# Optimization experiments

Hardware: AMD Instinct MI355X
Metric: run time of the kernel (lower is better)

The kernel has to match this reference:

```python
import jax, jax.numpy as jnp
import numpy as np

NEG_SLOPE = 0.01  # F.leaky_relu default
BN_EPS = 1e-5


def _nnconv_bn_lrelu(x, src, dst, ef, W_edge, b_edge, W_root, b_root, gamma, beta):
    # PyG NNConv (aggr='add'): msg_e = x_src[e] @ reshape(nn(edge_feat[e]), [in, out])
    E = ef.shape[0]
    in_c = x.shape[1]
    out_c = W_root.shape[1]
    We = (ef @ W_edge.T + b_edge).reshape(E, in_c, out_c)   # [E, in, out]
    msg = jnp.einsum('ei,eio->eo', x[src], We)               # gather + per-edge matvec
    aggr = jax.ops.segment_sum(msg, dst, num_segments=x.shape[0])  # scatter-add
    h = aggr + x @ W_root + b_root
    # BatchNorm1d in training mode: batch statistics over nodes (biased var)
    mean = jnp.mean(h, axis=0)
    var = jnp.var(h, axis=0)
    hn = (h - mean) * jax.lax.rsqrt(var + BN_EPS) * gamma + beta
    return jnp.where(hn > 0, hn, NEG_SLOPE * hn)             # LeakyReLU


def setup_inputs() -> dict:
    key = jax.random.key(0)
    ks = jax.random.split(key, 12)
    N, E = 8192, 32768
    D_NODE, D_EDGE, H, OUT = 64, 64, 64, 128
    node_features = jax.random.normal(ks[0], (N, D_NODE), dtype=jnp.float32)
    edge_index = jax.random.randint(ks[1], (2, E), 0, N, dtype=jnp.int32)
    edge_features = jax.random.normal(ks[2], (E, D_EDGE), dtype=jnp.float32)
    batch = jnp.zeros((N,), dtype=jnp.int32)
    s = 0.05
    params = {
        # layer 0: node_feats=D_NODE, edge_feats=D_EDGE, out=H
        'W_edge0': jax.random.normal(ks[3], (D_NODE * H, D_EDGE), dtype=jnp.float32) * s,
        'b_edge0': jnp.zeros((D_NODE * H,), dtype=jnp.float32),
        'W_root0': jax.random.normal(ks[4], (D_NODE, H), dtype=jnp.float32) * s,
        'b_root0': jnp.zeros((H,), dtype=jnp.float32),
        'gamma0': jnp.ones((H,), dtype=jnp.float32),
        'beta0': jnp.zeros((H,), dtype=jnp.float32),
        # layer 1: node_feats=H, edge_feats=H(==D_EDGE), out=H
        'W_edge1': jax.random.normal(ks[5], (H * H, D_EDGE), dtype=jnp.float32) * s,
        'b_edge1': jnp.zeros((H * H,), dtype=jnp.float32),
        'W_root1': jax.random.normal(ks[6], (H, H), dtype=jnp.float32) * s,
        'b_root1': jnp.zeros((H,), dtype=jnp.float32),
        'gamma1': jnp.ones((H,), dtype=jnp.float32),
        'beta1': jnp.zeros((H,), dtype=jnp.float32),
        # final linear
        'W_lin': jax.random.normal(ks[7], (OUT, H), dtype=jnp.float32) * s,
        'b_lin': jnp.zeros((OUT,), dtype=jnp.float32),
    }
    return {'node_features': node_features, 'edge_index': edge_index,
            'edge_features': edge_features, 'batch': batch, **params}


def reference(node_features, edge_index, edge_features, batch,
              W_edge0, b_edge0, W_root0, b_root0, gamma0, beta0,
              W_edge1, b_edge1, W_root1, b_root1, gamma1, beta1,
              W_lin, b_lin):
    src, dst = edge_index[0], edge_index[1]
    h = _nnconv_bn_lrelu(node_features, src, dst, edge_features,
                         W_edge0, b_edge0, W_root0, b_root0, gamma0, beta0)
    h = _nnconv_bn_lrelu(h, src, dst, edge_features,
                         W_edge1, b_edge1, W_root1, b_root1, gamma1, beta1)
    # dropout treated as identity (eval-mode determinism)
    return h @ W_lin.T + b_lin
```

## Files before the change

kernel.cpp:

```cpp
#include <hip/hip_runtime.h>

typedef __bf16 bf16x8 __attribute__((ext_vector_type(8)));
typedef float f32x4 __attribute__((ext_vector_type(4)));

#define NEG_SLOPE 0.01f
#define BN_EPS 1e-5f

static __device__ __forceinline__ unsigned short f2bf(float f) {
    unsigned u = __builtin_bit_cast(unsigned, f);
    unsigned r = (u + 0x7fffu + ((u >> 16) & 1u)) >> 16;
    return (unsigned short)r;
}
static __device__ __forceinline__ float bf2f(unsigned short s) {
    return __builtin_bit_cast(float, (unsigned)s << 16);
}
static __device__ __forceinline__ float lrelu(float v) {
    return fmaxf(v, 0.f) + NEG_SLOPE * fminf(v, 0.f);
}
static __device__ __forceinline__ f32x4 bn4(f32x4 v, f32x4 sc, f32x4 sh) {
    f32x4 r = v * sc + sh;
    r.x = lrelu(r.x); r.y = lrelu(r.y); r.z = lrelu(r.z); r.w = lrelu(r.w);
    return r;
}

__global__ __launch_bounds__(256) void prep(const float* __restrict__ We0,
                                            const float* __restrict__ We1,
                                            unsigned short* __restrict__ wbs0,
                                            unsigned short* __restrict__ wbs1,
                                            float* __restrict__ stats,
                                            const int* __restrict__ dst,
                                            int* __restrict__ hist, int E) {
    const int idx = blockIdx.x * 256 + threadIdx.x;
    if (blockIdx.x == 0) stats[threadIdx.x] = 0.f;
    if (idx < 65536) {
        const int t = idx;
        const float* We = (t >> 15) ? We1 : We0;
        unsigned short* wbs = (t >> 15) ? wbs1 : wbs0;
        const int r = t & 32767;
        const int i = r >> 9, os = (r >> 7) & 3, h = (r >> 6) & 1, l = r & 63;
        const float* sp = We + (size_t)(i * 64 + 16 * os + (l & 15)) * 64
                             + h * 32 + 8 * (l >> 4);
        const f32x4 v0 = *reinterpret_cast<const f32x4*>(sp);
        const f32x4 v1 = *reinterpret_cast<const f32x4*>(sp + 4);
        ushort4 u0, u1;
        u0.x = f2bf(v0.x); u0.y = f2bf(v0.y); u0.z = f2bf(v0.z); u0.w = f2bf(v0.w);
        u1.x = f2bf(v1.x); u1.y = f2bf(v1.y); u1.z = f2bf(v1.z); u1.w = f2bf(v1.w);
        *reinterpret_cast<ushort4*>(wbs + (size_t)r * 8) = u0;
        *reinterpret_cast<ushort4*>(wbs + (size_t)r * 8 + 4) = u1;
    } else {
        const int e = idx - 65536;
        if (e < E) atomicAdd(&hist[dst[e]], 1);
    }
}

__global__ __launch_bounds__(256) void scan_kernel(const int* __restrict__ hist,
                                                   int* __restrict__ ofs,
                                                   int* __restrict__ cur, int N) {
    __shared__ int wsum[4];
    const int tid = threadIdx.x;
    const int per = N / 256;
    const int base = tid * per;
    int loc[32];
    int s = 0;
#pragma unroll
    for (int k = 0; k < 32; ++k) { loc[k] = s; s += hist[base + k]; }
    const int lane = tid & 63, w = tid >> 6;
    int run = s;
#pragma unroll
    for (int d = 1; d < 64; d <<= 1) {
        int up = __shfl_up(run, d, 64);
        if (lane >= d) run += up;
    }
    const int excl = run - s;
    if (lane == 63) wsum[w] = run;
    __syncthreads();
    int woff = 0;
#pragma unroll
    for (int i = 0; i < 4; ++i) woff += (i < w) ? wsum[i] : 0;
    if (tid == 255) ofs[N] = woff + run;
    const int off = woff + excl;
#pragma unroll
    for (int k = 0; k < 32; ++k) {
        ofs[base + k] = off + loc[k];
        cur[base + k] = off + loc[k];
    }
}

__global__ __launch_bounds__(256) void scatter_reorder(
    const int* __restrict__ dst, const int* __restrict__ src,
    const float* __restrict__ ef, int* __restrict__ cur,
    unsigned short* __restrict__ ef_bs, int* __restrict__ src_s) {
    const int e = blockIdx.x * 256 + threadIdx.x;
    const int p = atomicAdd(&cur[dst[e]], 1);
    src_s[p] = src[e];
    const float* er = ef + (size_t)e * 64;
    unsigned short* orow = ef_bs + (size_t)p * 64;
#pragma unroll
    for (int c = 0; c < 16; ++c) {
        const f32x4 v = *reinterpret_cast<const f32x4*>(er + 4 * c);
        ushort4 u;
        u.x = f2bf(v.x); u.y = f2bf(v.y); u.z = f2bf(v.z); u.w = f2bf(v.w);
        *reinterpret_cast<ushort4*>(orow + 4 * c) = u;
    }
}

__global__ __launch_bounds__(256) void node_mm2(
    const float* __restrict__ x,
    const float* __restrict__ Wr, const float* __restrict__ br,
    const float* __restrict__ be,
    float* __restrict__ aggr, float* __restrict__ NB,
    const float* __restrict__ sums, const float* __restrict__ gamma,
    const float* __restrict__ beta, float invN) {
    __shared__ float Ml[64][64];
    __shared__ float Bl[64][64];
    __shared__ float xl[64][64];
    __shared__ float ssl[128];
    const int tid = threadIdx.x;
    if (sums) {
        if (tid < 64) {
            const float mean = sums[tid] * invN;
            const float var  = sums[64 + tid] * invN - mean * mean;
            const float sc = gamma[tid] * rsqrtf(var + BN_EPS);
            ssl[tid] = sc;
            ssl[64 + tid] = beta[tid] - mean * sc;
        }
        __syncthreads();
    }
    const int n0 = blockIdx.x * 64;
    for (int f = tid; f < 1024; f += 256) {
        int r = f >> 4, c = f & 15;
        *reinterpret_cast<float4*>(&Ml[r][c * 4]) =
            *reinterpret_cast<const float4*>(Wr + (size_t)r * 64 + c * 4);
        *reinterpret_cast<float4*>(&Bl[r][c * 4]) =
            *reinterpret_cast<const float4*>(be + (size_t)r * 64 + c * 4);
        f32x4 xv = *reinterpret_cast<const f32x4*>(x + (size_t)(n0 + r) * 64 + c * 4);
        if (sums) {
            const f32x4 sc = *reinterpret_cast<const f32x4*>(&ssl[c * 4]);
            const f32x4 sh = *reinterpret_cast<const f32x4*>(&ssl[64 + c * 4]);
            xv = bn4(xv, sc, sh);
        }
        *reinterpret_cast<f32x4*>(&xl[r][c * 4]) = xv;
    }
    __syncthreads();
    const int o = tid & 63, g = tid >> 6;
    float accA[16] = {}, accB[16] = {};
    for (int i4 = 0; i4 < 16; ++i4) {
        float m0 = Ml[4 * i4 + 0][o], m1 = Ml[4 * i4 + 1][o];
        float m2 = Ml[4 * i4 + 2][o], m3 = Ml[4 * i4 + 3][o];
        float b0 = Bl[4 * i4 + 0][o], b1 = Bl[4 * i4 + 1][o];
        float b2 = Bl[4 * i4 + 2][o], b3 = Bl[4 * i4 + 3][o];
#pragma unroll
        for (int k = 0; k < 16; ++k) {
            const f32x4 xv = *reinterpret_cast<const f32x4*>(&xl[g + 4 * k][4 * i4]);
            accA[k] += xv.x * m0 + xv.y * m1 + xv.z * m2 + xv.w * m3;
            accB[k] += xv.x * b0 + xv.y * b1 + xv.z * b2 + xv.w * b3;
        }
    }
    const float b = br[o];
#pragma unroll
    for (int k = 0; k < 16; ++k) {
        aggr[(size_t)(n0 + g + 4 * k) * 64 + o] = accA[k] + b;
        NB[(size_t)(n0 + g + 4 * k) * 64 + o]   = accB[k];
    }
}

__global__ __launch_bounds__(512, 1) void msg_fused(
    const unsigned short* __restrict__ ef_bs,
    const unsigned short* __restrict__ wbs,
    const float* __restrict__ x,
    const float* __restrict__ NB,
    const int* __restrict__ src_s,
    unsigned short* __restrict__ msg,
    const float* __restrict__ sums, const float* __restrict__ gamma,
    const float* __restrict__ beta, float invN) {
    __shared__ unsigned short wlds[32768];
    __shared__ float xT2[8192];
    __shared__ float ssl[128];
    const int tid = threadIdx.x;
    const int e0 = blockIdx.x * 128;
    if (sums) {
        if (tid < 64) {
            const float mean = sums[tid] * invN;
            const float var  = sums[64 + tid] * invN - mean * mean;
            const float sc = gamma[tid] * rsqrtf(var + BN_EPS);
            ssl[tid] = sc;
            ssl[64 + tid] = beta[tid] - mean * sc;
        }
        __syncthreads();
    }

#pragma unroll
    for (int it = 0; it < 4; ++it) {
        int f = it * 512 + tid;
        int e = f & 127, c = f >> 7;
        int s = src_s[e0 + e];
        f32x4 xv = *reinterpret_cast<const f32x4*>(x + (size_t)s * 64 + c * 4);
        if (sums) {
            const f32x4 sc = *reinterpret_cast<const f32x4*>(&ssl[c * 4]);
            const f32x4 sh = *reinterpret_cast<const f32x4*>(&ssl[64 + c * 4]);
            xv = bn4(xv, sc, sh);
        }
        const int base = (e >> 6) * 64 + (e & 15) * 4 + ((e >> 4) & 3);
        xT2[(4 * c + 0) * 128 + base] = xv.x;
        xT2[(4 * c + 1) * 128 + base] = xv.y;
        xT2[(4 * c + 2) * 128 + base] = xv.z;
        xT2[(4 * c + 3) * 128 + base] = xv.w;
    }

    const int w = tid >> 6, l = tid & 63, lg = l >> 4, ln = l & 15;
    const int os = w & 3, eh = w >> 2;

    bf16x8 B0[4], B1[4];
#pragma unroll
    for (int tt = 0; tt < 4; ++tt) {
        const unsigned short* pe = ef_bs + (size_t)(e0 + 64 * eh + 16 * tt + ln) * 64 + 8 * lg;
        B0[tt] = *reinterpret_cast<const bf16x8*>(pe);
        B1[tt] = *reinterpret_cast<const bf16x8*>(pe + 32);
    }

    const char* gW = (const char*)wbs;
    char* wldsB = (char*)wlds;
#define GLD(c, j) (*reinterpret_cast<const bf16x8*>(gW + (size_t)(c) * 32768 + (j) * 8192 + tid * 16))
#define SST(b, j, v) (*reinterpret_cast<bf16x8*>(wldsB + (b) * 32768 + (j) * 8192 + tid * 16) = (v))

    bf16x8 S0 = GLD(0, 0), S1 = GLD(0, 1), S2 = GLD(0, 2), S3 = GLD(0, 3);
    SST(0, 0, S0); SST(0, 1, S1); SST(0, 2, S2); SST(0, 3, S3);
    S0 = GLD(1, 0); S1 = GLD(1, 1); S2 = GLD(1, 2); S3 = GLD(1, 3);
    __syncthreads();

    f32x4 acc[4] = {};
    const int wofs = os * 1024 + l * 8;
    for (int t = 0; t < 16; ++t) {
        const unsigned short* wb_ = wlds + (t & 1) * 16384 + wofs;
#pragma unroll
        for (int ii = 0; ii < 4; ++ii) {
            const bf16x8 A0 = *reinterpret_cast<const bf16x8*>(wb_ + ii * 4096);
            const bf16x8 A1 = *reinterpret_cast<const bf16x8*>(wb_ + ii * 4096 + 512);
            const f32x4 xs = *reinterpret_cast<const f32x4*>(
                &xT2[(t * 4 + ii) * 128 + eh * 64 + ln * 4]);
#pragma unroll
            for (int tt = 0; tt < 4; ++tt) {
                f32x4 c = {};
                c = __builtin_amdgcn_mfma_f32_16x16x32_bf16(A0, B0[tt], c, 0, 0, 0);
                c = __builtin_amdgcn_mfma_f32_16x16x32_bf16(A1, B1[tt], c, 0, 0, 0);
                acc[tt] += xs[tt] * c;
            }
        }
        if (t < 15) {
            const int nb = (t + 1) & 1;
            SST(nb, 0, S0); SST(nb, 1, S1); SST(nb, 2, S2); SST(nb, 3, S3);
            if (t < 14) {
                S0 = GLD(t + 2, 0); S1 = GLD(t + 2, 1);
                S2 = GLD(t + 2, 2); S3 = GLD(t + 2, 3);
            }
        }
        __syncthreads();
    }
#undef GLD
#undef SST

#pragma unroll
    for (int tt = 0; tt < 4; ++tt) {
        const int e = e0 + 64 * eh + 16 * tt + ln;
        const int s = src_s[e];
        const f32x4 nbv = *reinterpret_cast<const f32x4*>(NB + (size_t)s * 64 + os * 16 + 4 * lg);
        const f32x4 add = acc[tt] + nbv;
        ushort4 u;
        u.x = f2bf(add.x); u.y = f2bf(add.y); u.z = f2bf(add.z); u.w = f2bf(add.w);
        *reinterpret_cast<ushort4*>(msg + (size_t)e * 64 + os * 16 + 4 * lg) = u;
    }
}

__global__ __launch_bounds__(256) void gather_k(const unsigned short* __restrict__ msg,
                                                const int* __restrict__ ofs,
                                                float* __restrict__ aggr) {
    const int tid = threadIdx.x;
    const int w = tid >> 6, lane = tid & 63;
    const int v = blockIdx.x * 4 + w;
    const int beg = ofs[v], end = ofs[v + 1];
    float a0 = 0.f, a1 = 0.f, a2 = 0.f, a3 = 0.f;
    int j = beg;
    for (; j + 4 <= end; j += 4) {
        a0 += bf2f(msg[(size_t)(j + 0) * 64 + lane]);
        a1 += bf2f(msg[(size_t)(j + 1) * 64 + lane]);
        a2 += bf2f(msg[(size_t)(j + 2) * 64 + lane]);
        a3 += bf2f(msg[(size_t)(j + 3) * 64 + lane]);
    }
    for (; j < end; ++j) a0 += bf2f(msg[(size_t)j * 64 + lane]);
    aggr[(size_t)v * 64 + lane] += (a0 + a1) + (a2 + a3);
}

__global__ __launch_bounds__(256) void bn_stats(const float* __restrict__ h,
                                                float* __restrict__ sums) {
    const int tid = threadIdx.x;
    const int o = tid & 63, g = tid >> 6;
    const int n0 = blockIdx.x * 128;
    float s = 0.f, s2 = 0.f;
    for (int k = 0; k < 32; ++k) {
        float v = h[(size_t)(n0 + g * 32 + k) * 64 + o];
        s += v; s2 += v * v;
    }
    __shared__ float red[2][4][64];
    red[0][g][o] = s; red[1][g][o] = s2;
    __syncthreads();
    if (g == 0) {
        s  = red[0][0][o] + red[0][1][o] + red[0][2][o] + red[0][3][o];
        s2 = red[1][0][o] + red[1][1][o] + red[1][2][o] + red[1][3][o];
        atomicAdd(&sums[o], s);
        atomicAdd(&sums[64 + o], s2);
    }
}

__global__ __launch_bounds__(256) void out_kernel(
    const float* __restrict__ x2, const float* __restrict__ Wl,
    const float* __restrict__ bl, float* __restrict__ out,
    const float* __restrict__ sums, const float* __restrict__ gamma,
    const float* __restrict__ beta, float invN) {
    __shared__ float Wt[64][129];
    __shared__ float xl[64][64];
    __shared__ float ssl[128];
    const int tid = threadIdx.x;
    if (tid < 64) {
        const float mean = sums[tid] * invN;
        const float var  = sums[64 + tid] * invN - mean * mean;
        const float sc = gamma[tid] * rsqrtf(var + BN_EPS);
        ssl[tid] = sc;
        ssl[64 + tid] = beta[tid] - mean * sc;
    }
    __syncthreads();
    const int n0 = blockIdx.x * 64;
    for (int f = tid; f < 8192; f += 256) {
        int q = f >> 6, o = f & 63;
        Wt[o][q] = Wl[f];
    }
    for (int f = tid; f < 1024; f += 256) {
        int r = f >> 4, c = f & 15;
        f32x4 xv = *reinterpret_cast<const f32x4*>(x2 + (size_t)(n0 + r) * 64 + c * 4);
        const f32x4 sc = *reinterpret_cast<const f32x4*>(&ssl[c * 4]);
        const f32x4 sh = *reinterpret_cast<const f32x4*>(&ssl[64 + c * 4]);
        xv = bn4(xv, sc, sh);
        *reinterpret_cast<f32x4*>(&xl[r][c * 4]) = xv;
    }
    __syncthreads();
    const int q = tid & 127, ng = tid >> 7;
    float acc[32] = {};
    for (int o4 = 0; o4 < 16; ++o4) {
        float w0 = Wt[4 * o4 + 0][q], w1 = Wt[4 * o4 + 1][q];
        float w2 = Wt[4 * o4 + 2][q], w3 = Wt[4 * o4 + 3][q];
#pragma unroll
        for (int k = 0; k < 32; ++k) {
            const f32x4 xv = *reinterpret_cast<const f32x4*>(&xl[ng + 2 * k][4 * o4]);
            acc[k] += xv.x * w0 + xv.y * w1 + xv.z * w2 + xv.w * w3;
        }
    }
    const float b = bl[q];
#pragma unroll
    for (int k = 0; k < 32; ++k)
        out[(size_t)(n0 + ng + 2 * k) * 128 + q] = acc[k] + b;
}

extern "C" void kernel_launch(void* const* d_in, const int* in_sizes, int n_in,
                              void* d_out, int out_size, void* d_ws, size_t ws_size,
                              hipStream_t stream) {
    const float* nf      = (const float*)d_in[0];
    const int*   ei      = (const int*)d_in[1];
    const float* ef      = (const float*)d_in[2];
    const float* W_edge0 = (const float*)d_in[4];
    const float* b_edge0 = (const float*)d_in[5];
    const float* W_root0 = (const float*)d_in[6];
    const float* b_root0 = (const float*)d_in[7];
    const float* gamma0  = (const float*)d_in[8];
    const float* beta0   = (const float*)d_in[9];
    const float* W_edge1 = (const float*)d_in[10];
    const float* b_edge1 = (const float*)d_in[11];
    const float* W_root1 = (const float*)d_in[12];
    const float* b_root1 = (const float*)d_in[13];
    const float* gamma1  = (const float*)d_in[14];
    const float* beta1   = (const float*)d_in[15];
    const float* W_lin   = (const float*)d_in[16];
    const float* b_lin   = (const float*)d_in[17];

    const int N = in_sizes[0] / 64;
    const int E = in_sizes[1] / 2;
    const int* src = ei;
    const int* dst = ei + E;

    unsigned short* ef_bs = (unsigned short*)d_ws;
    unsigned short* wbs0  = ef_bs + (size_t)E * 64;
    unsigned short* wbs1  = wbs0 + 262144;
    unsigned short* msg   = wbs1 + 262144;
    float* aggr0 = (float*)(msg + (size_t)E * 64);
    float* aggr1 = aggr0 + (size_t)N * 64;
    float* NBbuf = aggr1 + (size_t)N * 64;
    float* stats = NBbuf + (size_t)N * 64;
    int*   hist  = (int*)(stats + 256);
    int*   ofs   = hist + N;
    int*   cur   = ofs + N + 1;
    int*   src_s = cur + N;

    const float invN = 1.0f / (float)N;

    hipMemsetAsync(hist, 0, N * sizeof(int), stream);
    prep<<<(65536 + E) / 256, 256, 0, stream>>>(W_edge0, W_edge1, wbs0, wbs1,
                                                stats, dst, hist, E);
    scan_kernel<<<1, 256, 0, stream>>>(hist, ofs, cur, N);
    scatter_reorder<<<E / 256, 256, 0, stream>>>(dst, src, ef, cur, ef_bs, src_s);

    node_mm2<<<N / 64, 256, 0, stream>>>(nf, W_root0, b_root0, b_edge0, aggr0, NBbuf,
                                         nullptr, nullptr, nullptr, invN);
    msg_fused<<<E / 128, 512, 0, stream>>>(ef_bs, wbs0, nf, NBbuf, src_s, msg,
                                           nullptr, nullptr, nullptr, invN);
    gather_k<<<N / 4, 256, 0, stream>>>(msg, ofs, aggr0);
    bn_stats<<<N / 128, 256, 0, stream>>>(aggr0, stats);

    node_mm2<<<N / 64, 256, 0, stream>>>(aggr0, W_root1, b_root1, b_edge1, aggr1, NBbuf,
                                         stats, gamma0, beta0, invN);
    msg_fused<<<E / 128, 512, 0, stream>>>(ef_bs, wbs1, aggr0, NBbuf, src_s, msg,
                                           stats, gamma0, beta0, invN);
    gather_k<<<N / 4, 256, 0, stream>>>(msg, ofs, aggr1);
    bn_stats<<<N / 128, 256, 0, stream>>>(aggr1, stats + 128);

    out_kernel<<<N / 64, 256, 0, stream>>>(aggr1, W_lin, b_lin, (float*)d_out,
                                           stats + 128, gamma1, beta1, invN);
}
```

Baseline: 126.7 us.

## Precompute normalized bf16 node features and halve msg_fused tile to 64 edges

node_mm2 now writes a bf16 copy of the (batch-normalized) node features, so msg_fused gathers half the bytes and no longer recomputes BN scale/shift per block. msg_fused is retiled to 64 edges per 256-thread block with two blocks per CU, giving twice as many blocks. The gathered x is stored as padded bf16 rows in LDS and converted per step. Each block still streams the full 512 KB edge-weight matrix, so total weight traffic from L2 doubles. The x multiplier is also rounded to bf16, which costs some precision.

Result: slower. 129.7 us (+2.4%).

```diff
diff --git a/kernel.cpp b/kernel.cpp
--- a/kernel.cpp
+++ b/kernel.cpp
@@ -109,6 +109,7 @@
     const float* __restrict__ Wr, const float* __restrict__ br,
     const float* __restrict__ be,
     float* __restrict__ aggr, float* __restrict__ NB,
+    unsigned short* __restrict__ xb,
     const float* __restrict__ sums, const float* __restrict__ gamma,
     const float* __restrict__ beta, float invN) {
     __shared__ float Ml[64][64];
@@ -140,6 +141,9 @@
             xv = bn4(xv, sc, sh);
         }
         *reinterpret_cast<f32x4*>(&xl[r][c * 4]) = xv;
+        ushort4 u;
+        u.x = f2bf(xv.x); u.y = f2bf(xv.y); u.z = f2bf(xv.z); u.w = f2bf(xv.w);
+        *reinterpret_cast<ushort4*>(xb + (size_t)(n0 + r) * 64 + c * 4) = u;
     }
     __syncthreads();
     const int o = tid & 63, g = tid >> 6;
@@ -164,94 +168,86 @@
     }
 }
 
-__global__ __launch_bounds__(512, 1) void msg_fused(
+__global__ __launch_bounds__(256, 2) void msg_fused(
     const unsigned short* __restrict__ ef_bs,
     const unsigned short* __restrict__ wbs,
-    const float* __restrict__ x,
+    const unsigned short* __restrict__ xb,
     const float* __restrict__ NB,
     const int* __restrict__ src_s,
-    unsigned short* __restrict__ msg,
-    const float* __restrict__ sums, const float* __restrict__ gamma,
-    const float* __restrict__ beta, float invN) {
+    unsigned short* __restrict__ msg) {
     __shared__ unsigned short wlds[32768];
-    __shared__ float xT2[8192];
-    __shared__ float ssl[128];
-    const int tid = threadIdx.x;
-    const int e0 = blockIdx.x * 128;
-    if (sums) {
-        if (tid < 64) {
-            const float mean = sums[tid] * invN;
-            const float var  = sums[64 + tid] * invN - mean * mean;
-            const float sc = gamma[tid] * rsqrtf(var + BN_EPS);
-            ssl[tid] = sc;
-            ssl[64 + tid] = beta[tid] - mean * sc;
-        }
-        __syncthreads();
-    }
-
-#pragma unroll
-    for (int it = 0; it < 4; ++it) {
-        int f = it * 512 + tid;
-        int e = f & 127, c = f >> 7;
+    __shared__ unsigned short xT2[64 * 68];
+    const int tid = threadIdx.x;
+    const int e0 = blockIdx.x * 64;
+
+#pragma unroll
+    for (int it = 0; it < 2; ++it) {
+        int f = it * 256 + tid;
+        int e = f & 63, c8 = f >> 6;
         int s = src_s[e0 + e];
-        f32x4 xv = *reinterpret_cast<const f32x4*>(x + (size_t)s * 64 + c * 4);
-        if (sums) {
-            const f32x4 sc = *reinterpret_cast<const f32x4*>(&ssl[c * 4]);
-            const f32x4 sh = *reinterpret_cast<const f32x4*>(&ssl[64 + c * 4]);
-            xv = bn4(xv, sc, sh);
-        }
-        const int base = (e >> 6) * 64 + (e & 15) * 4 + ((e >> 4) & 3);
-        xT2[(4 * c + 0) * 128 + base] = xv.x;
-        xT2[(4 * c + 1) * 128 + base] = xv.y;
-        xT2[(4 * c + 2) * 128 + base] = xv.z;
-        xT2[(4 * c + 3) * 128 + base] = xv.w;
+        const ushort4 v0 = *reinterpret_cast<const ushort4*>(xb + (size_t)s * 64 + c8 * 8);
+        const ushort4 v1 = *reinterpret_cast<const ushort4*>(xb + (size_t)s * 64 + c8 * 8 + 4);
+        *reinterpret_cast<ushort4*>(&xT2[e * 68 + c8 * 8])     = v0;
+        *reinterpret_cast<ushort4*>(&xT2[e * 68 + c8 * 8 + 4]) = v1;
     }
 
     const int w = tid >> 6, l = tid & 63, lg = l >> 4, ln = l & 15;
-    const int os = w & 3, eh = w >> 2;
+    const int os = w;
 
     bf16x8 B0[4], B1[4];
 #pragma unroll
     for (int tt = 0; tt < 4; ++tt) {
-        const unsigned short* pe = ef_bs + (size_t)(e0 + 64 * eh + 16 * tt + ln) * 64 + 8 * lg;
+        const unsigned short* pe = ef_bs + (size_t)(e0 + 16 * tt + ln) * 64 + 8 * lg;
         B0[tt] = *reinterpret_cast<const bf16x8*>(pe);
         B1[tt] = *reinterpret_cast<const bf16x8*>(pe + 32);
     }
 
     const char* gW = (const char*)wbs;
     char* wldsB = (char*)wlds;
-#define GLD(c, j) (*reinterpret_cast<const bf16x8*>(gW + (size_t)(c) * 32768 + (j) * 8192 + tid * 16))
-#define SST(b, j, v) (*reinterpret_cast<bf16x8*>(wldsB + (b) * 32768 + (j) * 8192 + tid * 16) = (v))
+#define GLD(c, j) (*reinterpret_cast<const bf16x8*>(gW + (size_t)(c) * 32768 + (j) * 4096 + tid * 16))
+#define SST(b, j, v) (*reinterpret_cast<bf16x8*>(wldsB + (b) * 32768 + (j) * 4096 + tid * 16) = (v))
 
     bf16x8 S0 = GLD(0, 0), S1 = GLD(0, 1), S2 = GLD(0, 2), S3 = GLD(0, 3);
+    bf16x8 S4 = GLD(0, 4), S5 = GLD(0, 5), S6 = GLD(0, 6), S7 = GLD(0, 7);
     SST(0, 0, S0); SST(0, 1, S1); SST(0, 2, S2); SST(0, 3, S3);
+    SST(0, 4, S4); SST(0, 5, S5); SST(0, 6, S6); SST(0, 7, S7);
     S0 = GLD(1, 0); S1 = GLD(1, 1); S2 = GLD(1, 2); S3 = GLD(1, 3);
+    S4 = GLD(1, 4); S5 = GLD(1, 5); S6 = GLD(1, 6); S7 = GLD(1, 7);
     __syncthreads();
 
     f32x4 acc[4] = {};
     const int wofs = os * 1024 + l * 8;
     for (int t = 0; t < 16; ++t) {
         const unsigned short* wb_ = wlds + (t & 1) * 16384 + wofs;
+        f32x4 xsv[4];
+#pragma unroll
+        for (int tt = 0; tt < 4; ++tt) {
+            const ushort4 xu = *reinterpret_cast<const ushort4*>(
+                &xT2[(16 * tt + ln) * 68 + 4 * t]);
+            xsv[tt].x = bf2f(xu.x); xsv[tt].y = bf2f(xu.y);
+            xsv[tt].z = bf2f(xu.z); xsv[tt].w = bf2f(xu.w);
+        }
 #pragma unroll
         for (int ii = 0; ii < 4; ++ii) {
             const bf16x8 A0 = *reinterpret_cast<const bf16x8*>(wb_ + ii * 4096);
             const bf16x8 A1 = *reinterpret_cast<const bf16x8*>(wb_ + ii * 4096 + 512);
-            const f32x4 xs = *reinterpret_cast<const f32x4*>(
-                &xT2[(t * 4 + ii) * 128 + eh * 64 + ln * 4]);
 #pragma unroll
             for (int tt = 0; tt < 4; ++tt) {
                 f32x4 c = {};
                 c = __builtin_amdgcn_mfma_f32_16x16x32_bf16(A0, B0[tt], c, 0, 0, 0);
                 c = __builtin_amdgcn_mfma_f32_16x16x32_bf16(A1, B1[tt], c, 0, 0, 0);
-                acc[tt] += xs[tt] * c;
+                acc[tt] += xsv[tt][ii] * c;
             }
         }
         if (t < 15) {
             const int nb = (t + 1) & 1;
             SST(nb, 0, S0); SST(nb, 1, S1); SST(nb, 2, S2); SST(nb, 3, S3);
+            SST(nb, 4, S4); SST(nb, 5, S5); SST(nb, 6, S6); SST(nb, 7, S7);
             if (t < 14) {
                 S0 = GLD(t + 2, 0); S1 = GLD(t + 2, 1);
                 S2 = GLD(t + 2, 2); S3 = GLD(t + 2, 3);
+                S4 = GLD(t + 2, 4); S5 = GLD(t + 2, 5);
+                S6 = GLD(t + 2, 6); S7 = GLD(t + 2, 7);
             }
         }
         __syncthreads();
@@ -261,7 +257,7 @@
 
 #pragma unroll
     for (int tt = 0; tt < 4; ++tt) {
-        const int e = e0 + 64 * eh + 16 * tt + ln;
+        const int e = e0 + 16 * tt + ln;
         const int s = src_s[e];
         const f32x4 nbv = *reinterpret_cast<const f32x4*>(NB + (size_t)s * 64 + os * 16 + 4 * lg);
         const f32x4 add = acc[tt] + nbv;
@@ -389,7 +385,8 @@
     unsigned short* wbs0  = ef_bs + (size_t)E * 64;
     unsigned short* wbs1  = wbs0 + 262144;
     unsigned short* msg   = wbs1 + 262144;
-    float* aggr0 = (float*)(msg + (size_t)E * 64);
+    unsigned short* xbuf  = msg + (size_t)E * 64;
+    float* aggr0 = (float*)(xbuf + (size_t)N * 64);
     float* aggr1 = aggr0 + (size_t)N * 64;
     float* NBbuf = aggr1 + (size_t)N * 64;
     float* stats = NBbuf + (size_t)N * 64;
@@ -407,16 +404,14 @@
     scatter_reorder<<<E / 256, 256, 0, stream>>>(dst, src, ef, cur, ef_bs, src_s);
 
     node_mm2<<<N / 64, 256, 0, stream>>>(nf, W_root0, b_root0, b_edge0, aggr0, NBbuf,
-                                         nullptr, nullptr, nullptr, invN);
-    msg_fused<<<E / 128, 512, 0, stream>>>(ef_bs, wbs0, nf, NBbuf, src_s, msg,
-                                           nullptr, nullptr, nullptr, invN);
+                                         xbuf, nullptr, nullptr, nullptr, invN);
+    msg_fused<<<E / 64, 256, 0, stream>>>(ef_bs, wbs0, xbuf, NBbuf, src_s, msg);
     gather_k<<<N / 4, 256, 0, stream>>>(msg, ofs, aggr0);
     bn_stats<<<N / 128, 256, 0, stream>>>(aggr0, stats);
 
     node_mm2<<<N / 64, 256, 0, stream>>>(aggr0, W_root1, b_root1, b_edge1, aggr1, NBbuf,
-                                         stats, gamma0, beta0, invN);
-    msg_fused<<<E / 128, 512, 0, stream>>>(ef_bs, wbs1, aggr0, NBbuf, src_s, msg,
-                                           stats, gamma0, beta0, invN);
+                                         xbuf, stats, gamma0, beta0, invN);
+    msg_fused<<<E / 64, 256, 0, stream>>>(ef_bs, wbs1, xbuf, NBbuf, src_s, msg);
     gather_k<<<N / 4, 256, 0, stream>>>(msg, ofs, aggr1);
     bn_stats<<<N / 128, 256, 0, stream>>>(aggr1, stats + 128);
 
```
